# Kernel tuning notes

Hardware: AMD Instinct MI355X
Metric: run time of the kernel (lower is better)

The kernel has to match this reference:

```python
import jax, jax.numpy as jnp
import numpy as np

B, S, DIM = 2, 2048, 2048
H = 16
KV_RANK = 512
D_NOPE, D_ROPE, D_V = 128, 64, 128
QK_HEAD = D_NOPE + D_ROPE  # 192
THETA = 10000.0


def make_freqs(seqlen, d_rope, theta=THETA):
    inv = 1.0 / (theta ** (np.arange(0, d_rope, 2, dtype=np.float32) / d_rope))
    ang = np.outer(np.arange(seqlen, dtype=np.float32), inv)  # [S, d/2]
    return jnp.asarray(np.cos(ang)), jnp.asarray(np.sin(ang))


def apply_rope(x, cos, sin):
    # x: [b, s, h, d]; cos/sin: [s, d//2]; complex-pair rotation (interleaved pairs)
    xr = x.reshape(*x.shape[:-1], -1, 2)
    re, im = xr[..., 0], xr[..., 1]
    c = cos[None, :, None, :]
    s = sin[None, :, None, :]
    out = jnp.stack([re * c - im * s, re * s + im * c], axis=-1)
    return out.reshape(x.shape)


def setup_inputs() -> dict:
    key = jax.random.key(0)
    ks = jax.random.split(key, 6)
    w_scale = 0.02
    cos, sin = make_freqs(S, D_ROPE)
    return {
        'x': jax.random.normal(ks[0], (B, S, DIM), dtype=jnp.float32),
        'freqs_cos': cos,
        'freqs_sin': sin,
        'wq': jax.random.normal(ks[1], (H * QK_HEAD, DIM), dtype=jnp.float32) * w_scale,
        'wkv_a': jax.random.normal(ks[2], (KV_RANK + D_ROPE, DIM), dtype=jnp.float32) * w_scale,
        'wkv_b': jax.random.normal(ks[3], (H * (D_NOPE + D_V), KV_RANK), dtype=jnp.float32) * w_scale,
        'wo': jax.random.normal(ks[4], (DIM, H * D_V), dtype=jnp.float32) * w_scale,
        'alpha': jnp.ones((1,), jnp.float32) * 0.5,
        'gamma': jnp.ones((KV_RANK,), jnp.float32),
        'beta': jnp.zeros((KV_RANK,), jnp.float32),
    }


def reference(x, freqs_cos, freqs_sin, wq, wkv_a, wkv_b, wo, alpha, gamma, beta):
    b, s, _ = x.shape
    # Q projection -> [b, s, h, qk_head]
    q = (x @ wq.T).reshape(b, s, H, QK_HEAD)
    q_nope, q_pe = q[..., :D_NOPE], q[..., D_NOPE:]
    q_pe = apply_rope(q_pe, freqs_cos, freqs_sin)

    # latent KV projection
    kv_full = x @ wkv_a.T                      # [b, s, kv_rank + d_rope]
    kv, k_pe = kv_full[..., :KV_RANK], kv_full[..., KV_RANK:]
    k_pe = apply_rope(k_pe[:, :, None, :], freqs_cos, freqs_sin)[:, :, 0, :]  # [b, s, d_rope]
    # DyT norm on latent kv
    kvn = jnp.tanh(alpha * kv) * gamma + beta  # [b, s, kv_rank]

    # absorbed attention: fold wkv_b into q and output
    wkv_b_h = wkv_b.reshape(H, D_NOPE + D_V, KV_RANK)
    wk = wkv_b_h[:, :D_NOPE]                   # [h, d_nope, c]
    wv = wkv_b_h[:, D_NOPE:]                   # [h, d_v, c]
    q_abs = jnp.einsum('bshd,hdc->bshc', q_nope, wk)  # [b, s, h, c]

    scale = QK_HEAD ** -0.5
    scores = (jnp.einsum('bshc,btc->bsht', q_abs, kvn)
              + jnp.einsum('bshr,btr->bsht', q_pe, k_pe)) * scale
    probs = jax.nn.softmax(scores, axis=-1)

    o_lat = jnp.einsum('bsht,btc->bshc', probs, kvn)          # latent-space output
    o = jnp.einsum('bshc,hdc->bshd', o_lat, wv)               # [b, s, h, d_v]
    return o.reshape(b, s, H * D_V) @ wo.T
```

## Files before the change

### kernel.cpp

```cpp
#include <hip/hip_runtime.h>
#include <math.h>

typedef __bf16 bf16x8 __attribute__((ext_vector_type(8)));
typedef float f32x4 __attribute__((ext_vector_type(4)));

#define LOG2E 1.4426950408889634f

__device__ __forceinline__ unsigned short bf16r(float f) {
  unsigned u = __float_as_uint(f);
  u = (u + 0x7fffu + ((u >> 16) & 1u)) >> 16;
  return (unsigned short)u;
}
__device__ __forceinline__ unsigned short bfc(float f) {
  __bf16 h = (__bf16)f;
  return __builtin_bit_cast(unsigned short, h);
}
__device__ __forceinline__ float bf2f(unsigned short h) {
  return __uint_as_float(((unsigned)h) << 16);
}

#define GLOAD16(gsrc, ldst)                                                        \
  __builtin_amdgcn_global_load_lds(                                                \
      (const __attribute__((address_space(1))) void*)(gsrc),                       \
      (__attribute__((address_space(3))) void*)(ldst), 16, 0, 0)

__device__ __forceinline__ void map_block(int& bx, int& by, int& z) {
  const int gx = gridDim.x, gy = gridDim.y;
  const int nwg = gx * gy * gridDim.z;
  int id = blockIdx.x + gx * (blockIdx.y + gy * blockIdx.z);
  if (gridDim.z == 1 && (gx & 3) == 0 && (gy & 1) == 0 && (nwg & 7) == 0) {
    const int xcd = id & 7, k = id >> 3;
    const int rx = gx >> 2, ry = gy >> 1;
    bx = (xcd & 3) * rx + (k % rx);
    by = (xcd >> 2) * ry + (k / rx);
    z = 0;
  } else {
    if ((nwg & 7) == 0) id = (id & 7) * (nwg >> 3) + (id >> 3);
    bx = id % gx;
    const int t1 = id / gx;
    by = t1 % gy;
    z = t1 / gy;
  }
}

__global__ void conv_all(const float* __restrict__ x, const float* __restrict__ wq,
                         const float* __restrict__ wkva, const float* __restrict__ wkvb,
                         const float* __restrict__ wo,
                         unsigned short* __restrict__ xb, unsigned short* __restrict__ wqb,
                         unsigned short* __restrict__ wab, unsigned short* __restrict__ wbb,
                         unsigned short* __restrict__ wob) {
  int bid = blockIdx.x;
  const float* src; unsigned short* dst; long nsrc;
  if (bid < 8192)       {               src = x;    dst = xb;  nsrc = 8388608; }
  else if (bid < 14336) { bid -= 8192;  src = wq;   dst = wqb; nsrc = 6291456; }
  else if (bid < 15616) { bid -= 14336; src = wkva; dst = wab; nsrc = 1179648; }
  else if (bid < 17664) { bid -= 15616; src = wkvb; dst = wbb; nsrc = 2097152; }
  else                  { bid -= 17664; src = wo;   dst = wob; nsrc = 4194304; }
  long i = ((long)bid * 256 + threadIdx.x) * 4;
  ushort4 o;
  if (i < nsrc) {
    float4 v = *(const float4*)&src[i];
    o.x = bf16r(v.x); o.y = bf16r(v.y); o.z = bf16r(v.z); o.w = bf16r(v.w);
  } else {
    o.x = 0; o.y = 0; o.z = 0; o.w = 0;
  }
  *(ushort4*)&dst[i] = o;
}

template <int BN, int MODE>
__global__ __launch_bounds__(512) void gemm8p(
    const unsigned short* __restrict__ A, const unsigned short* __restrict__ B,
    void* __restrict__ Cv, float* __restrict__ laux,
    int Mrows, int K, int lda, int ldb, int ldc, int zs,
    long sAh, long sAl, long sBh, long sBl, long sCh, long sCl, float alpha)
{
  constexpr int BM = 256;
  constexpr int WN = BN / 4;
  constexpr int NR = WN / 16;
  constexpr int BU = BN / 64;
  constexpr int BU1 = (BU + 1) / 2;

  __shared__ unsigned short As[2][BM * 64];
  __shared__ unsigned short Bs[2][BN * 64];

  const int tid = threadIdx.x;
  const int w = tid >> 6, l = tid & 63, lg = l & 15, lh = l >> 4;
  const int wmi = w >> 2, wni = w & 3;
  const int lrow = l >> 3;
  const int swz8 = ((l & 7) ^ lrow) * 8;

  int bx, by, z;
  map_block(bx, by, z);
  const int zh = z >> zs, zl = z & ((1 << zs) - 1);

  const unsigned short* Ab = A + zh * sAh + zl * sAl + (long)(bx * BM) * lda;
  const unsigned short* Bb = B + zh * sBh + zl * sBl + (long)(by * BN) * ldb;

  const int nt = K >> 6;

  auto stA = [&](int T, int u) {
    if (T >= nt) return;
    const int rr = u * 64 + w * 8;
    GLOAD16(Ab + (long)(rr + lrow) * lda + (T << 6) + swz8, &As[T & 1][rr * 64]);
  };
  auto stB = [&](int T, int u) {
    if (T >= nt) return;
    const int rr = u * 64 + w * 8;
    GLOAD16(Bb + (long)(rr + lrow) * ldb + (T << 6) + swz8, &Bs[T & 1][rr * 64]);
  };

  stA(0, 0); stA(0, 1); stA(0, 2); stA(0, 3);
#pragma unroll
  for (int u = 0; u < BU; ++u) stB(0, u);
  stA(1, 0); stA(1, 2);

  f32x4 acc[8][NR] = {};

  const int nit = nt >> 1;
  for (int i = 0; i < nit; ++i) {
    const int t0 = 2 * i;
#pragma unroll
    for (int j = 0; j < 8; ++j) {
      const int tau = t0 + (j >> 2);
      const int jj = j & 3;
      const int mh = jj & 1, kh = jj >> 1;
      if (jj == 0) {
        if (tau + 1 < nt) asm volatile("s_waitcnt vmcnt(2)" ::: "memory");
        else              asm volatile("s_waitcnt vmcnt(0)" ::: "memory");
      } else {
        asm volatile("" ::: "memory");
      }
      __builtin_amdgcn_s_barrier();
      if (j == 0)      { stA(t0 + 1, 1); stA(t0 + 1, 3); }
      else if (j == 1) { for (int u = 0; u < BU1; ++u) stB(t0 + 1, u); }
      else if (j == 2) { for (int u = BU1; u < BU; ++u) stB(t0 + 1, u); }
      else if (j == 3) { stA(t0 + 2, 0); stA(t0 + 2, 2); }
      else if (j == 4) { stA(t0 + 2, 1); stA(t0 + 2, 3); }
      else if (j == 5) { for (int u = 0; u < BU1; ++u) stB(t0 + 2, u); }
      else if (j == 6) { for (int u = BU1; u < BU; ++u) stB(t0 + 2, u); }
      else             { stA(t0 + 3, 0); stA(t0 + 3, 2); }
      const unsigned short* bA = As[tau & 1];
      const unsigned short* bB = Bs[tau & 1];
      const int rswz = ((kh * 4 + lh) ^ (lg & 7)) * 8;
      bf16x8 af[4], bf[NR];
#pragma unroll
      for (int mi = 0; mi < 4; ++mi)
        af[mi] = *(const bf16x8*)&bA[(wmi * 128 + mh * 64 + mi * 16 + lg) * 64 + rswz];
#pragma unroll
      for (int ni = 0; ni < NR; ++ni)
        bf[ni] = *(const bf16x8*)&bB[(wni * WN + ni * 16 + lg) * 64 + rswz];
      __builtin_amdgcn_s_setprio(1);
#pragma unroll
      for (int mi = 0; mi < 4; ++mi)
#pragma unroll
        for (int ni = 0; ni < NR; ++ni)
          acc[mh * 4 + mi][ni] = __builtin_amdgcn_mfma_f32_16x16x32_bf16(
              af[mi], bf[ni], acc[mh * 4 + mi][ni], 0, 0, 0);
      __builtin_amdgcn_s_setprio(0);
    }
  }

  if (nt & 1) {
    const int tau = nt - 1;
    asm volatile("s_waitcnt vmcnt(0)" ::: "memory");
    __builtin_amdgcn_s_barrier();
    const unsigned short* bA = As[tau & 1];
    const unsigned short* bB = Bs[tau & 1];
#pragma unroll
    for (int jj = 0; jj < 4; ++jj) {
      const int mh = jj & 1, kh = jj >> 1;
      const int rswz = ((kh * 4 + lh) ^ (lg & 7)) * 8;
      bf16x8 af[4], bf[NR];
#pragma unroll
      for (int mi = 0; mi < 4; ++mi)
        af[mi] = *(const bf16x8*)&bA[(wmi * 128 + mh * 64 + mi * 16 + lg) * 64 + rswz];
#pragma unroll
      for (int ni = 0; ni < NR; ++ni)
        bf[ni] = *(const bf16x8*)&bB[(wni * WN + ni * 16 + lg) * 64 + rswz];
      __builtin_amdgcn_s_setprio(1);
#pragma unroll
      for (int mi = 0; mi < 4; ++mi)
#pragma unroll
        for (int ni = 0; ni < NR; ++ni)
          acc[mh * 4 + mi][ni] = __builtin_amdgcn_mfma_f32_16x16x32_bf16(
              af[mi], bf[ni], acc[mh * 4 + mi][ni], 0, 0, 0);
      __builtin_amdgcn_s_setprio(0);
    }
  }

  const int row0 = bx * BM + wmi * 128;
  const int col0 = by * BN + wni * WN;
  const long coff = (long)zh * sCh + (long)zl * sCl;

  if (MODE == 4) {
#pragma unroll
    for (int mi = 0; mi < 8; ++mi)
#pragma unroll
      for (int r = 0; r < 4; ++r) {
        const int row = row0 + mi * 16 + lh * 4 + r;
        unsigned short* dq = (unsigned short*)Cv +
            (long)(row >> 11) * 6291456 + (long)by * 393216 + (long)(row & 2047) * 192;
#pragma unroll
        for (int ni = 0; ni < NR; ++ni)
          dq[wni * WN + ni * 16 + lg] = bf16r(acc[mi][ni][r] * alpha);
      }
  } else {
#pragma unroll
    for (int mi = 0; mi < 8; ++mi)
#pragma unroll
      for (int r = 0; r < 4; ++r) {
        const int row = row0 + mi * 16 + lh * 4 + r;
#pragma unroll
        for (int ni = 0; ni < NR; ++ni) {
          float v = acc[mi][ni][r] * alpha;
          if (MODE == 0)
            ((float*)Cv)[coff + (long)row * ldc + col0 + ni * 16 + lg] = v;
          else
            ((unsigned short*)Cv)[coff + (long)row * ldc + col0 + ni * 16 + lg] = bf16r(v);
        }
      }
  }
}

template <int MODE>
__global__ __launch_bounds__(256) void gemm4w(
    const unsigned short* __restrict__ A, const unsigned short* __restrict__ B,
    void* __restrict__ Cv, float* __restrict__ laux,
    int Mrows, int K, int lda, int ldb, int ldc, int zs,
    long sAh, long sAl, long sBh, long sBl, long sCh, long sCl, float alpha)
{
  constexpr int BM = 128, BN = 128, WN = 64, NR = 4;

  __shared__ unsigned short As[2][BM * 64];
  __shared__ unsigned short Bs[2][BN * 64];

  const int tid = threadIdx.x;
  const int w = tid >> 6, l = tid & 63, lg = l & 15, lh = l >> 4;
  const int wmi = w >> 1, wni = w & 1;
  const int lrow = l >> 3;
  const int swz8 = ((l & 7) ^ lrow) * 8;

  int bx, by, z;
  map_block(bx, by, z);
  const int zh = z >> zs, zl = z & ((1 << zs) - 1);

  const unsigned short* Ab = A + zh * sAh + zl * sAl + (long)(bx * BM) * lda;
  const unsigned short* Bb = B + zh * sBh + zl * sBl + (long)(by * BN) * ldb;

  const int nt = K >> 6;

  auto stage = [&](int T) {
    const int k0 = T << 6;
    const int d = T & 1;
#pragma unroll
    for (int u = 0; u < 4; ++u) {
      const int rr = u * 32 + w * 8;
      GLOAD16(Ab + (long)(rr + lrow) * lda + k0 + swz8, &As[d][rr * 64]);
    }
#pragma unroll
    for (int u = 0; u < 4; ++u) {
      const int rr = u * 32 + w * 8;
      GLOAD16(Bb + (long)(rr + lrow) * ldb + k0 + swz8, &Bs[d][rr * 64]);
    }
  };

  f32x4 acc[4][NR] = {};

  stage(0);
  for (int t = 0; t < nt; ++t) {
    asm volatile("s_waitcnt vmcnt(0)" ::: "memory");
    __builtin_amdgcn_s_barrier();
    if (t + 1 < nt) stage(t + 1);
    const unsigned short* bA = As[t & 1];
    const unsigned short* bB = Bs[t & 1];
#pragma unroll
    for (int kh = 0; kh < 2; ++kh) {
      const int rswz = ((kh * 4 + lh) ^ (lg & 7)) * 8;
      bf16x8 af[4], bf[NR];
#pragma unroll
      for (int mi = 0; mi < 4; ++mi)
        af[mi] = *(const bf16x8*)&bA[(wmi * 64 + mi * 16 + lg) * 64 + rswz];
#pragma unroll
      for (int ni = 0; ni < NR; ++ni)
        bf[ni] = *(const bf16x8*)&bB[(wni * WN + ni * 16 + lg) * 64 + rswz];
      __builtin_amdgcn_s_setprio(1);
#pragma unroll
      for (int mi = 0; mi < 4; ++mi)
#pragma unroll
        for (int ni = 0; ni < NR; ++ni)
          acc[mi][ni] = __builtin_amdgcn_mfma_f32_16x16x32_bf16(
              af[mi], bf[ni], acc[mi][ni], 0, 0, 0);
      __builtin_amdgcn_s_setprio(0);
    }
  }

  const int row0 = bx * BM + wmi * 64;
  const int col0 = by * BN + wni * WN;
  const long coff = (long)zh * sCh + (long)zl * sCl;

#pragma unroll
  for (int mi = 0; mi < 4; ++mi)
#pragma unroll
    for (int r = 0; r < 4; ++r) {
      const int row = row0 + mi * 16 + lh * 4 + r;
#pragma unroll
      for (int ni = 0; ni < NR; ++ni) {
        float v = acc[mi][ni][r] * alpha;
        if (MODE == 0)
          ((float*)Cv)[coff + (long)row * ldc + col0 + ni * 16 + lg] = v;
        else
          ((unsigned short*)Cv)[coff + (long)row * ldc + col0 + ni * 16 + lg] = bf16r(v);
      }
    }
}

__global__ __launch_bounds__(256, 2) void attn_fused(
    const unsigned short* __restrict__ q192, const unsigned short* __restrict__ kh,
    const unsigned short* __restrict__ vhT, unsigned short* __restrict__ o_b)
{
  __shared__ unsigned short Ks[2][3 * 64 * 64];
  __shared__ unsigned short Ps[64 * 72];

  const int tid = threadIdx.x;
  const int w = tid >> 6, l = tid & 63, lg = l & 15, lh = l >> 4;
  const int wmi = w >> 1, wni = w & 1;
  const int lrow = l >> 3;
  const int swz8 = ((l & 7) ^ lrow) * 8;

  int id = blockIdx.x;
  id = (id & 7) * 128 + (id >> 3);
  const int bx = id & 31;
  const int z = id >> 5;
  const int b = z >> 4, hh = z & 15;

  const unsigned short* Qg = q192 + (long)z * 393216 + (long)(bx * 64) * 192;
  const unsigned short* Kg = kh + (long)z * 393216;
  const unsigned short* Vg = vhT + (long)z * 262144;

  bf16x8 qf[2][6];
#pragma unroll
  for (int mi = 0; mi < 2; ++mi)
#pragma unroll
    for (int s = 0; s < 6; ++s)
      qf[mi][s] = *(const bf16x8*)&Qg[(wmi * 32 + mi * 16 + lg) * 192 + s * 32 + lh * 8];

  bf16x8 ones;
#pragma unroll
  for (int j = 0; j < 8; ++j) ((unsigned short*)&ones)[j] = 0x3F80;

  auto stageK = [&](int T) {
    if (T >= 32) return;
    const unsigned short* src = Kg + (long)(T * 64) * 192;
    unsigned short* dst = Ks[T & 1];
#pragma unroll
    for (int u = 0; u < 3; ++u)
#pragma unroll
      for (int i = 0; i < 2; ++i) {
        const int rr = w * 16 + i * 8;
        GLOAD16(src + (long)(rr + lrow) * 192 + u * 64 + swz8, &dst[u * 4096 + rr * 64]);
      }
  };
  auto loadV = [&](int T, bf16x8 (&vf)[8]) {
    if (T >= 32) return;
#pragma unroll
    for (int j = 0; j < 8; ++j)
      vf[j] = *(const bf16x8*)&Vg[(long)(wni * 64 + (j & 3) * 16 + lg) * 2048 +
                                  T * 64 + (j >> 2) * 32 + lh * 8];
  };

  f32x4 acc_o[2][4] = {};
  f32x4 accl[2] = {};
  bf16x8 vfA[8], vfB[8];

  stageK(0);
  loadV(0, vfA);

  auto tile = [&](int t, bf16x8 (&vcur)[8], bf16x8 (&vnext)[8]) {
    asm volatile("s_waitcnt vmcnt(0)" ::: "memory");
    __builtin_amdgcn_s_barrier();
    stageK(t + 1);
    loadV(t + 1, vnext);
    const unsigned short* bK = Ks[t & 1];

    f32x4 acc_s[2][2] = {};
#pragma unroll
    for (int u = 0; u < 3; ++u) {
      bf16x8 kf[4];
#pragma unroll
      for (int half = 0; half < 2; ++half) {
        const int rswz = ((half * 4 + lh) ^ (lg & 7)) * 8;
#pragma unroll
        for (int n = 0; n < 2; ++n)
          kf[half * 2 + n] =
              *(const bf16x8*)&bK[u * 4096 + (wni * 32 + n * 16 + lg) * 64 + rswz];
      }
      __builtin_amdgcn_s_setprio(1);
#pragma unroll
      for (int half = 0; half < 2; ++half)
#pragma unroll
        for (int mi = 0; mi < 2; ++mi)
#pragma unroll
          for (int n = 0; n < 2; ++n)
            acc_s[mi][n] = __builtin_amdgcn_mfma_f32_16x16x32_bf16(
                qf[mi][u * 2 + half], kf[half * 2 + n], acc_s[mi][n], 0, 0, 0);
      __builtin_amdgcn_s_setprio(0);
    }
#pragma unroll
    for (int mi = 0; mi < 2; ++mi)
#pragma unroll
      for (int n = 0; n < 2; ++n)
#pragma unroll
        for (int r = 0; r < 4; ++r)
          Ps[(wmi * 32 + mi * 16 + lh * 4 + r) * 72 + wni * 32 + n * 16 + lg] =
              bfc(exp2f(acc_s[mi][n][r] * LOG2E));
    __builtin_amdgcn_s_barrier();

#pragma unroll
    for (int k2 = 0; k2 < 2; ++k2) {
      bf16x8 pf[2];
#pragma unroll
      for (int mi = 0; mi < 2; ++mi)
        pf[mi] = *(const bf16x8*)&Ps[(wmi * 32 + mi * 16 + lg) * 72 + k2 * 32 + lh * 8];
      __builtin_amdgcn_s_setprio(1);
#pragma unroll
      for (int mi = 0; mi < 2; ++mi) {
        accl[mi] = __builtin_amdgcn_mfma_f32_16x16x32_bf16(pf[mi], ones, accl[mi], 0, 0, 0);
#pragma unroll
        for (int n = 0; n < 4; ++n)
          acc_o[mi][n] = __builtin_amdgcn_mfma_f32_16x16x32_bf16(
              pf[mi], vcur[k2 * 4 + n], acc_o[mi][n], 0, 0, 0);
      }
      __builtin_amdgcn_s_setprio(0);
    }
  };

  for (int tt = 0; tt < 16; ++tt) {
    tile(2 * tt, vfA, vfB);
    tile(2 * tt + 1, vfB, vfA);
  }

#pragma unroll
  for (int mi = 0; mi < 2; ++mi)
#pragma unroll
    for (int r = 0; r < 4; ++r) {
      const int row = bx * 64 + wmi * 32 + mi * 16 + lh * 4 + r;
      const float inv = 1.0f / accl[mi][r];
      unsigned short* dst = o_b + (long)(b * 2048 + row) * 2048 + hh * 128 + wni * 64;
#pragma unroll
      for (int n = 0; n < 4; ++n)
        dst[n * 16 + lg] = bfc(acc_o[mi][n][r] * inv);
    }
}

template <int MODE>
__global__ __launch_bounds__(256) void gemm_bt2(
    const unsigned short* __restrict__ A, const unsigned short* __restrict__ B,
    void* __restrict__ Cv, float* __restrict__ laux,
    int M, int Nstore, int K, int lda, int ldb, int ldc, int zs,
    long sAh, long sAl, long sBh, long sBl, long sCh, long sCl, float alpha)
{
  __shared__ unsigned short As[128 * 32];
  __shared__ unsigned short Bs[128 * 32];
  const int tid = threadIdx.x;
  const int w = tid >> 6, l = tid & 63, lg = l & 15, lh = l >> 4;

  int bx, by, z;
  map_block(bx, by, z);

  const int zh = z >> zs, zl = z & ((1 << zs) - 1);
  const unsigned short* Ab = A + zh * sAh + zl * sAl + (long)(bx * 128) * lda;
  const unsigned short* Bb = B + zh * sBh + zl * sBl + (long)(by * 128) * ldb;
  const int srow = l >> 2;
  const int scol = (((l & 3) ^ ((l >> 3) & 3)) * 8);
  const int wm = (w >> 1) * 64, wn = (w & 1) * 64;
  f32x4 acc[4][4] = {};

  const long ra0 = (long)(w * 16 + srow) * lda + scol;
  const long ra1 = (long)(64 + w * 16 + srow) * lda + scol;
  const long rb0 = (long)(w * 16 + srow) * ldb + scol;
  const long rb1 = (long)(64 + w * 16 + srow) * ldb + scol;
  unsigned short* lA0 = &As[(w * 16) * 32];
  unsigned short* lA1 = &As[(64 + w * 16) * 32];
  unsigned short* lB0 = &Bs[(w * 16) * 32];
  unsigned short* lB1 = &Bs[(64 + w * 16) * 32];

  const int rsw = ((lh ^ ((lg >> 1) & 3)) * 8);

  for (int k0 = 0; k0 < K; k0 += 32) {
    __syncthreads();
    GLOAD16(Ab + ra0 + k0, lA0);
    GLOAD16(Ab + ra1 + k0, lA1);
    GLOAD16(Bb + rb0 + k0, lB0);
    GLOAD16(Bb + rb1 + k0, lB1);
    __syncthreads();
    bf16x8 af[4], bfr[4];
#pragma unroll
    for (int m = 0; m < 4; m++) af[m] = *(const bf16x8*)&As[(wm + m * 16 + lg) * 32 + rsw];
#pragma unroll
    for (int n = 0; n < 4; n++) bfr[n] = *(const bf16x8*)&Bs[(wn + n * 16 + lg) * 32 + rsw];
#pragma unroll
    for (int m = 0; m < 4; m++)
#pragma unroll
      for (int n = 0; n < 4; n++)
        acc[m][n] = __builtin_amdgcn_mfma_f32_16x16x32_bf16(af[m], bfr[n], acc[m][n], 0, 0, 0);
  }

  const int row0 = bx * 128 + wm, col0 = by * 128 + wn;
  long coff = zh * sCh + zl * sCl;

#pragma unroll
  for (int m = 0; m < 4; m++)
#pragma unroll
    for (int r = 0; r < 4; r++) {
      const int row = row0 + m * 16 + lh * 4 + r;
#pragma unroll
      for (int n = 0; n < 4; n++) {
        int col = col0 + n * 16 + lg;
        if (col < Nstore) {
          float v = acc[m][n][r] * alpha;
          if (MODE == 0)
            ((float*)Cv)[coff + (long)row * ldc + col] = v;
          else
            ((unsigned short*)Cv)[coff + (long)row * ldc + col] = bf16r(v);
        }
      }
    }
}

__global__ void kv_epilogue(const float* __restrict__ kvf, const float* __restrict__ fc,
                            const float* __restrict__ fs, const float* __restrict__ alpha,
                            const float* __restrict__ gamma, const float* __restrict__ beta,
                            unsigned short* __restrict__ kvn, unsigned short* __restrict__ kh) {
  const int n = blockIdx.x;
  const int b = n >> 11, s = n & 2047;
  const int tid = threadIdx.x;
  const float a = alpha[0];
  const float* src = kvf + (long)n * 576;
  unsigned short* dst = kvn + (long)n * 512;
#pragma unroll
  for (int c0 = 0; c0 < 512; c0 += 256) {
    int c = c0 + tid;
    float v = tanhf(a * src[c]) * gamma[c] + beta[c];
    dst[c] = bf16r(v);
  }
  if (tid < 32) {
    int i = tid;
    float re = src[512 + 2 * i], im = src[512 + 2 * i + 1];
    float co = fc[s * 32 + i], si = fs[s * 32 + i];
    ushort2 v;
    v.x = bf16r(re * co - im * si);
    v.y = bf16r(re * si + im * co);
#pragma unroll
    for (int h = 0; h < 16; h++)
      *(ushort2*)&kh[((long)(b * 16 + h) * 2048 + s) * 192 + 128 + 2 * i] = v;
  }
}

__global__ void q_ropefix(unsigned short* __restrict__ q192, const float* __restrict__ fc,
                          const float* __restrict__ fs) {
  const int n = blockIdx.x;
  const int b = n >> 11, s = n & 2047;
  const int tid = threadIdx.x;
  for (int it = tid; it < 512; it += 256) {
    int h = it >> 5, i = it & 31;
    unsigned short* dd = q192 + ((long)(b * 16 + h) * 2048 + s) * 192 + 128 + 2 * i;
    float re = bf2f(dd[0]), im = bf2f(dd[1]);
    float co = fc[s * 32 + i], si = fs[s * 32 + i];
    ushort2 o;
    o.x = bf16r(re * co - im * si);
    o.y = bf16r(re * si + im * co);
    *(ushort2*)dd = o;
  }
}

extern "C" void kernel_launch(void* const* d_in, const int* in_sizes, int n_in,
                              void* d_out, int out_size, void* d_ws, size_t ws_size,
                              hipStream_t stream) {
  const float* x = (const float*)d_in[0];
  const float* fc = (const float*)d_in[1];
  const float* fs = (const float*)d_in[2];
  const float* wq = (const float*)d_in[3];
  const float* wkva = (const float*)d_in[4];
  const float* wkvb = (const float*)d_in[5];
  const float* wo = (const float*)d_in[6];
  const float* alpha = (const float*)d_in[7];
  const float* gamma = (const float*)d_in[8];
  const float* beta = (const float*)d_in[9];
  float* out = (float*)d_out;

  char* p = (char*)d_ws;
  auto take = [&](size_t bytes) {
    char* r = p;
    p += (bytes + 255) & ~(size_t)255;
    return r;
  };
  unsigned short* wqb   = (unsigned short*)take(6291456ull * 2);
  float*          kvf   = (float*)take(2359296ull * 4);
  unsigned short* xb    = (unsigned short*)take(8388608ull * 2);
  unsigned short* wab   = (unsigned short*)take(1310720ull * 2);
  unsigned short* wbb   = (unsigned short*)take(2097152ull * 2);
  unsigned short* wob   = (unsigned short*)take(4194304ull * 2);
  unsigned short* kvn   = (unsigned short*)take(2097152ull * 2);
  unsigned short* kh    = (unsigned short*)take(12582912ull * 2);
  unsigned short* q192  = (unsigned short*)take(12582912ull * 2);
  unsigned short* vhT   = (unsigned short*)take(8388608ull * 2);
  unsigned short* o_b   = (unsigned short*)take(8388608ull * 2);

  const float scale = 1.0f / sqrtf(192.0f);

  conv_all<<<21760, 256, 0, stream>>>(x, wq, wkva, wkvb, wo, xb, wqb, wab, wbb, wob);

  gemm8p<192, 4><<<dim3(16, 16, 1), 512, 0, stream>>>(
      xb, wqb, q192, nullptr, 4096, 2048, 2048, 2048, 192, 0, 0, 0, 0, 0, 0, 0, scale);
  gemm_bt2<0><<<dim3(32, 5, 1), 256, 0, stream>>>(xb, wab, kvf, nullptr, 4096, 576, 2048,
                                                  2048, 2048, 576, 0, 0, 0, 0, 0, 0, 0, 1.0f);
  kv_epilogue<<<4096, 256, 0, stream>>>(kvf, fc, fs, alpha, gamma, beta, kvn, kh);
  gemm4w<1><<<dim3(16, 1, 32), 256, 0, stream>>>(
      kvn, wbb, kh, nullptr, 2048, 512, 512, 512, 192, 4,
      1048576, 0, 0, 131072, 6291456, 393216, 1.0f);
  q_ropefix<<<4096, 256, 0, stream>>>(q192, fc, fs);
  gemm4w<1><<<dim3(1, 16, 32), 256, 0, stream>>>(
      wbb + 128 * 512, kvn, vhT, nullptr, 128, 512, 512, 512, 2048, 4,
      0, 131072, 1048576, 0, 4194304, 262144, 1.0f);

  attn_fused<<<1024, 256, 0, stream>>>(q192, kh, vhT, o_b);

  gemm4w<0><<<dim3(32, 16, 1), 256, 0, stream>>>(
      o_b, wob, out, nullptr, 4096, 2048, 2048, 2048, 2048, 0,
      0, 0, 0, 0, 0, 0, 1.0f);
}
```

Measured before the change: 369.1 us.

## Split attention tile across eight waves and drop V register double-buffering

The fused attention kernel now runs 512 threads (8 waves) per block instead of 256. Each wave owns a 32x16 slice of the score tile and a 32x32 slice of the output, so per-wave accumulators and K fragments are halved. The register double-buffered V prefetch is replaced by a plain load of V at the top of each tile, which frees registers for higher occupancy (launch bounds 512,4). The cost is that V load latency is no longer hidden behind the previous tile, each wave has less MFMA work between barriers, and Q fragments are now loaded redundantly by more waves.

```diff
diff --git a/kernel.cpp b/kernel.cpp
--- a/kernel.cpp
+++ b/kernel.cpp
@@ -314,7 +314,7 @@
     }
 }
 
-__global__ __launch_bounds__(256, 2) void attn_fused(
+__global__ __launch_bounds__(512, 4) void attn_fused(
     const unsigned short* __restrict__ q192, const unsigned short* __restrict__ kh,
     const unsigned short* __restrict__ vhT, unsigned short* __restrict__ o_b)
 {
@@ -323,7 +323,7 @@
 
   const int tid = threadIdx.x;
   const int w = tid >> 6, l = tid & 63, lg = l & 15, lh = l >> 4;
-  const int wmi = w >> 1, wni = w & 1;
+  const int wmi = w >> 2, wni = w & 3;
   const int lrow = l >> 3;
   const int swz8 = ((l & 7) ^ lrow) * 8;
 
@@ -353,66 +353,51 @@
     const unsigned short* src = Kg + (long)(T * 64) * 192;
     unsigned short* dst = Ks[T & 1];
 #pragma unroll
-    for (int u = 0; u < 3; ++u)
-#pragma unroll
-      for (int i = 0; i < 2; ++i) {
-        const int rr = w * 16 + i * 8;
-        GLOAD16(src + (long)(rr + lrow) * 192 + u * 64 + swz8, &dst[u * 4096 + rr * 64]);
-      }
+    for (int u = 0; u < 3; ++u) {
+      const int rr = w * 8;
+      GLOAD16(src + (long)(rr + lrow) * 192 + u * 64 + swz8, &dst[u * 4096 + rr * 64]);
+    }
   };
-  auto loadV = [&](int T, bf16x8 (&vf)[8]) {
-    if (T >= 32) return;
-#pragma unroll
-    for (int j = 0; j < 8; ++j)
-      vf[j] = *(const bf16x8*)&Vg[(long)(wni * 64 + (j & 3) * 16 + lg) * 2048 +
-                                  T * 64 + (j >> 2) * 32 + lh * 8];
-  };
-
-  f32x4 acc_o[2][4] = {};
+
+  f32x4 acc_o[2][2] = {};
   f32x4 accl[2] = {};
-  bf16x8 vfA[8], vfB[8];
 
   stageK(0);
-  loadV(0, vfA);
-
-  auto tile = [&](int t, bf16x8 (&vcur)[8], bf16x8 (&vnext)[8]) {
+  for (int t = 0; t < 32; ++t) {
     asm volatile("s_waitcnt vmcnt(0)" ::: "memory");
     __builtin_amdgcn_s_barrier();
+    bf16x8 vf[4];
+#pragma unroll
+    for (int j = 0; j < 4; ++j)
+      vf[j] = *(const bf16x8*)&Vg[(long)(wni * 32 + (j & 1) * 16 + lg) * 2048 +
+                                  t * 64 + (j >> 1) * 32 + lh * 8];
     stageK(t + 1);
-    loadV(t + 1, vnext);
     const unsigned short* bK = Ks[t & 1];
 
-    f32x4 acc_s[2][2] = {};
+    f32x4 acc_s[2] = {};
 #pragma unroll
     for (int u = 0; u < 3; ++u) {
-      bf16x8 kf[4];
+      bf16x8 kf[2];
 #pragma unroll
       for (int half = 0; half < 2; ++half) {
         const int rswz = ((half * 4 + lh) ^ (lg & 7)) * 8;
-#pragma unroll
-        for (int n = 0; n < 2; ++n)
-          kf[half * 2 + n] =
-              *(const bf16x8*)&bK[u * 4096 + (wni * 32 + n * 16 + lg) * 64 + rswz];
+        kf[half] = *(const bf16x8*)&bK[u * 4096 + (wni * 16 + lg) * 64 + rswz];
       }
       __builtin_amdgcn_s_setprio(1);
 #pragma unroll
       for (int half = 0; half < 2; ++half)
 #pragma unroll
         for (int mi = 0; mi < 2; ++mi)
-#pragma unroll
-          for (int n = 0; n < 2; ++n)
-            acc_s[mi][n] = __builtin_amdgcn_mfma_f32_16x16x32_bf16(
-                qf[mi][u * 2 + half], kf[half * 2 + n], acc_s[mi][n], 0, 0, 0);
+          acc_s[mi] = __builtin_amdgcn_mfma_f32_16x16x32_bf16(
+              qf[mi][u * 2 + half], kf[half], acc_s[mi], 0, 0, 0);
       __builtin_amdgcn_s_setprio(0);
     }
 #pragma unroll
     for (int mi = 0; mi < 2; ++mi)
 #pragma unroll
-      for (int n = 0; n < 2; ++n)
-#pragma unroll
-        for (int r = 0; r < 4; ++r)
-          Ps[(wmi * 32 + mi * 16 + lh * 4 + r) * 72 + wni * 32 + n * 16 + lg] =
-              bfc(exp2f(acc_s[mi][n][r] * LOG2E));
+      for (int r = 0; r < 4; ++r)
+        Ps[(wmi * 32 + mi * 16 + lh * 4 + r) * 72 + wni * 16 + lg] =
+            bfc(exp2f(acc_s[mi][r] * LOG2E));
     __builtin_amdgcn_s_barrier();
 
 #pragma unroll
@@ -426,17 +411,12 @@
       for (int mi = 0; mi < 2; ++mi) {
         accl[mi] = __builtin_amdgcn_mfma_f32_16x16x32_bf16(pf[mi], ones, accl[mi], 0, 0, 0);
 #pragma unroll
-        for (int n = 0; n < 4; ++n)
+        for (int n = 0; n < 2; ++n)
           acc_o[mi][n] = __builtin_amdgcn_mfma_f32_16x16x32_bf16(
-              pf[mi], vcur[k2 * 4 + n], acc_o[mi][n], 0, 0, 0);
+              pf[mi], vf[k2 * 2 + n], acc_o[mi][n], 0, 0, 0);
       }
       __builtin_amdgcn_s_setprio(0);
     }
-  };
-
-  for (int tt = 0; tt < 16; ++tt) {
-    tile(2 * tt, vfA, vfB);
-    tile(2 * tt + 1, vfB, vfA);
   }
 
 #pragma unroll
@@ -445,9 +425,9 @@
     for (int r = 0; r < 4; ++r) {
       const int row = bx * 64 + wmi * 32 + mi * 16 + lh * 4 + r;
       const float inv = 1.0f / accl[mi][r];
-      unsigned short* dst = o_b + (long)(b * 2048 + row) * 2048 + hh * 128 + wni * 64;
-#pragma unroll
-      for (int n = 0; n < 4; ++n)
+      unsigned short* dst = o_b + (long)(b * 2048 + row) * 2048 + hh * 128 + wni * 32;
+#pragma unroll
+      for (int n = 0; n < 2; ++n)
         dst[n * 16 + lg] = bfc(acc_o[mi][n][r] * inv);
     }
 }
@@ -623,7 +603,7 @@
       wbb + 128 * 512, kvn, vhT, nullptr, 128, 512, 512, 512, 2048, 4,
       0, 131072, 1048576, 0, 4194304, 262144, 1.0f);
 
-  attn_fused<<<1024, 256, 0, stream>>>(q192, kh, vhT, o_b);
+  attn_fused<<<1024, 512, 0, stream>>>(q192, kh, vhT, o_b);
 
   gemm4w<0><<<dim3(32, 16, 1), 256, 0, stream>>>(
       o_b, wob, out, nullptr, 4096, 2048, 2048, 2048, 2048, 0,
```

After: 357.1 us (median of 2 runs). 1.03x faster.
